# Performance work log

Hardware: AMD Instinct MI355X
Metric: run time of the kernel (lower is better)

## Reference

```python
import jax, jax.numpy as jnp
import numpy as np

B, N = 256, 256


def greedy_hard_perm(soft_perm):
    # soft_perm: (B, N, N). Sequential greedy masked-argmax assignment, vectorized over batch.
    Bn, Nn, _ = soft_perm.shape
    NEG = jnp.finfo(soft_perm.dtype).min
    b_idx = jnp.arange(Bn)

    def step(carry, _):
        scores, hard, row_mask, col_mask = carry
        # mask out already-assigned rows/cols (in-place masked_fill_ in torch -> carried scores)
        scores = jnp.where(row_mask[:, :, None], NEG, scores)
        scores = jnp.where(col_mask[:, None, :], NEG, scores)
        flat_idx = jnp.argmax(scores.reshape(Bn, -1), axis=1)  # (B,)
        r = flat_idx // Nn
        c = flat_idx % Nn
        hard = hard.at[b_idx, r, c].set(1.0)
        row_mask = row_mask.at[b_idx, r].set(True)
        col_mask = col_mask.at[b_idx, c].set(True)
        return (scores, hard, row_mask, col_mask), None

    init = (
        soft_perm,
        jnp.zeros_like(soft_perm),
        jnp.zeros((Bn, Nn), dtype=bool),
        jnp.zeros((Bn, Nn), dtype=bool),
    )
    (_, hard, _, _), _ = jax.lax.scan(step, init, None, length=Nn)
    return hard


def setup_inputs() -> dict:
    key = jax.random.key(0)
    logits = jax.random.normal(key, (B, N, N), dtype=jnp.float32)
    # realistic soft permutation: row-stochastic scores
    soft_perm = jax.nn.softmax(logits, axis=-1)
    return {"soft_perm": soft_perm}


def reference(soft_perm):
    # hard perm carries no gradient (built from constant 1.0 writes in torch)
    hard = greedy_hard_perm(jax.lax.stop_gradient(soft_perm))
    # straight-through estimator: forward = hard, backward = identity through soft
    return hard + soft_perm - jax.lax.stop_gradient(soft_perm)
```

## Files before the change

kernel.cpp:

```cpp
#include <hip/hip_runtime.h>
#include <math.h>

#define NEGINF (-INFINITY)
#define NEGINF_BITS ((int)0xFF800000)

typedef unsigned int u32;
typedef unsigned long long u64;

#define RST 128

template <int CTRL>
__device__ __forceinline__ float dppmax(float x) {
    int xi = __float_as_int(x);
    int yi = __builtin_amdgcn_update_dpp(xi, xi, CTRL, 0xf, 0xf, false);
    return fmaxf(x, __int_as_float(yi));
}

__device__ __forceinline__ float wave_max64(float x) {
    x = dppmax<0x111>(x);
    x = dppmax<0x112>(x);
    x = dppmax<0x114>(x);
    x = dppmax<0x118>(x);
    x = dppmax<0x142>(x);
    x = dppmax<0x143>(x);
    return __int_as_float(__builtin_amdgcn_readlane(__float_as_int(x), 63));
}

__device__ __forceinline__ void wave_argmax(float v, int idx, float& out_v, int& out_idx) {
    float mv = wave_max64(v);
    u64 mask = __ballot(v == mv);
    int ln = (int)__builtin_ctzll(mask);
    int bi = __builtin_amdgcn_readlane(idx, ln);
    u64 rest = mask & (mask - 1);
    if (rest) {
        while (rest) {
            int l2 = (int)__builtin_ctzll(rest); rest &= rest - 1;
            int b2 = __builtin_amdgcn_readlane(idx, l2);
            if (b2 < bi) bi = b2;
        }
    }
    out_v = mv; out_idx = bi;
}

__device__ __forceinline__ void wave_top2(float lv, int lf, float lv2, int lf2,
                                          float& nv, int& nc, float& nv2, int& nc2) {
    float av = lv, bv = lv2;
#define T2STAGE(CTRL) {                                                        \
        float a2 = __int_as_float(__builtin_amdgcn_update_dpp(                 \
            NEGINF_BITS, __float_as_int(av), CTRL, 0xf, 0xf, false));          \
        float b2 = __int_as_float(__builtin_amdgcn_update_dpp(                 \
            NEGINF_BITS, __float_as_int(bv), CTRL, 0xf, 0xf, false));          \
        float t = fminf(av, a2);                                               \
        av = fmaxf(av, a2);                                                    \
        bv = fmaxf(fmaxf(bv, b2), t); }
    T2STAGE(0x111) T2STAGE(0x112) T2STAGE(0x114) T2STAGE(0x118)
    T2STAGE(0x142) T2STAGE(0x143)
#undef T2STAGE
    nv = __int_as_float(__builtin_amdgcn_readlane(__float_as_int(av), 63));
    float sv = __int_as_float(__builtin_amdgcn_readlane(__float_as_int(bv), 63));

    u64 m1 = __ballot(lv == nv);
    int ln = (int)__builtin_ctzll(m1);
    nc = __builtin_amdgcn_readlane(lf, ln);

    nv2 = sv; nc2 = 300;
    if (sv > 0.f) {
        if (sv == nv) {
            int b2i = __builtin_amdgcn_readlane(__float_as_int(lv2), ln);
            if (__int_as_float(b2i) == nv) {
                nc2 = __builtin_amdgcn_readlane(lf2, ln);
            } else {
                u64 rest = m1 & (m1 - 1);
                int l2 = (int)__builtin_ctzll(rest);
                nc2 = __builtin_amdgcn_readlane(lf, l2);
            }
        } else {
            u64 m2 = __ballot(lv == sv || lv2 == sv);
            int l2 = (int)__builtin_ctzll(m2);
            int tli = __builtin_amdgcn_readlane(__float_as_int(lv), l2);
            nc2 = (__int_as_float(tli) == sv)
                      ? __builtin_amdgcn_readlane(lf, l2)
                      : __builtin_amdgcn_readlane(lf2, l2);
        }
    }
}

template <int RSTT>
__global__ __launch_bounds__(64, 1) void greedy_perm_kernel(
        const float* __restrict__ soft, float* __restrict__ out) {
    extern __shared__ float smem[];
    const int b = blockIdx.x;
    const int lane = threadIdx.x;
    const size_t base = (size_t)b << 16;
    const float* sc = soft + base;
    float* ob = out + base;

    float rv[4], sv[4];
    int   rc[4], scc[4];
#pragma unroll
    for (int j = 0; j < 4; ++j) { rv[j] = NEGINF; rc[j] = 0; sv[j] = NEGINF; scc[j] = 300; }

    const float4 zero4 = make_float4(0.f, 0.f, 0.f, 0.f);

    for (int k = 0; k < 64; k += 4) {
        float4 w[4][4];
#pragma unroll
        for (int j = 0; j < 4; ++j) {
            const float4* rp = (const float4*)(sc + (size_t)(j * 64 + lane) * 256);
#pragma unroll
            for (int kk = 0; kk < 4; ++kk) w[j][kk] = rp[k + kk];
        }
#pragma unroll
        for (int j = 0; j < 4; ++j) {
            float4* op = (float4*)(ob + (size_t)(j * 64 + lane) * 256);
#pragma unroll
            for (int kk = 0; kk < 4; ++kk) op[k + kk] = zero4;
        }
        if (RSTT > 0) {
#pragma unroll
            for (int j = 0; j < 2; ++j) {
                float* lp = &smem[(j * 64 + lane) << 8];
#pragma unroll
                for (int kk = 0; kk < 4; ++kk)
                    *(float4*)&lp[((k + kk) ^ lane) << 2] = w[j][kk];
            }
        }
#pragma unroll
        for (int j = 0; j < 4; ++j) {
#pragma unroll
            for (int kk = 0; kk < 4; ++kk) {
                const float4 ww = w[j][kk];
                const int bc = 4 * (k + kk);
                const float e[4] = {ww.x, ww.y, ww.z, ww.w};
#pragma unroll
                for (int q = 0; q < 4; ++q) {
                    const float x = e[q];
                    const int   cx = bc + q;
                    const bool g1 = x > rv[j];
                    const bool g2 = x > sv[j];
                    sv[j]  = g1 ? rv[j] : (g2 ? x  : sv[j]);
                    scc[j] = g1 ? rc[j] : (g2 ? cx : scc[j]);
                    rv[j]  = g1 ? x  : rv[j];
                    rc[j]  = g1 ? cx : rc[j];
                }
            }
        }
    }

    __threadfence_block();

    u32 colmask = 0;

    for (int step = 0; step < 256; ++step) {
        float bv = rv[0];
        int   bf = (lane << 8) | (rc[0] & 255);
#pragma unroll
        for (int j = 1; j < 4; ++j) {
            if (rv[j] > bv) { bv = rv[j]; bf = (((j << 6) + lane) << 8) | (rc[j] & 255); }
        }
        float gv; int gf;
        wave_argmax(bv, bf, gv, gf);
        (void)gv;
        const int r  = gf >> 8;
        const int cc = gf & 255;

        if (lane == 0) ob[gf] = 1.0f;
        if (lane == (r & 63)) {
            const int rj = r >> 6;
#pragma unroll
            for (int j = 0; j < 4; ++j) if (j == rj) { rv[j] = NEGINF; rc[j] = 300; }
        }
        if (lane == (cc >> 2)) colmask |= 1u << (cc & 3);

#pragma unroll
        for (int j = 0; j < 4; ++j) if (scc[j] == cc) scc[j] = 300;

        bool dd[4]; bool anyd = false;
#pragma unroll
        for (int j = 0; j < 4; ++j) { dd[j] = (rc[j] == cc); anyd |= dd[j]; }
        if (__ballot(anyd)) {
#pragma unroll
            for (int j = 0; j < 4; ++j) {
                const bool need = dd[j] && (scc[j] == 300);
                if (dd[j] && !need) {
                    rv[j] = sv[j]; rc[j] = scc[j];
                    sv[j] = NEGINF; scc[j] = 300;
                }
                u64 m = __ballot(need);
                while (m) {
                    const int ln = (int)__builtin_ctzll(m); m &= m - 1;
                    const int row = (j << 6) + ln;
                    float4 w = (RSTT > 0 && row < RSTT)
                        ? *(const float4*)&smem[(row << 8) | (((lane ^ ln) & 63) << 2)]
                        : *(const float4*)(sc + ((size_t)row << 8) + (lane << 2));
                    const float q0 = (colmask & 1u) ? NEGINF : w.x;
                    const float q1 = (colmask & 2u) ? NEGINF : w.y;
                    const float q2 = (colmask & 4u) ? NEGINF : w.z;
                    const float q3 = (colmask & 8u) ? NEGINF : w.w;
                    const int cb = lane << 2;
                    float lv = q0; int lf = cb;
                    float lv2 = NEGINF; int lf2 = cb;
                    {
                        bool g1 = q1 > lv, g2 = q1 > lv2;
                        lv2 = g1 ? lv : (g2 ? q1 : lv2); lf2 = g1 ? lf : (g2 ? cb + 1 : lf2);
                        lv  = g1 ? q1 : lv;              lf  = g1 ? cb + 1 : lf;
                        g1 = q2 > lv; g2 = q2 > lv2;
                        lv2 = g1 ? lv : (g2 ? q2 : lv2); lf2 = g1 ? lf : (g2 ? cb + 2 : lf2);
                        lv  = g1 ? q2 : lv;              lf  = g1 ? cb + 2 : lf;
                        g1 = q3 > lv; g2 = q3 > lv2;
                        lv2 = g1 ? lv : (g2 ? q3 : lv2); lf2 = g1 ? lf : (g2 ? cb + 3 : lf2);
                        lv  = g1 ? q3 : lv;              lf  = g1 ? cb + 3 : lf;
                    }
                    float nv, nv2; int nc, nc2;
                    wave_top2(lv, lf, lv2, lf2, nv, nc, nv2, nc2);
                    if (lane == ln) {
#pragma unroll
                        for (int jj = 0; jj < 4; ++jj) if (jj == j) {
                            rv[jj] = nv; rc[jj] = nc;
                            sv[jj] = nv2; scc[jj] = nc2;
                        }
                    }
                }
            }
        }
    }
}

extern "C" void kernel_launch(void* const* d_in, const int* in_sizes, int n_in,
                              void* d_out, int out_size, void* d_ws, size_t ws_size,
                              hipStream_t stream) {
    const float* soft = (const float*)d_in[0];
    float* out = (float*)d_out;
    const int n_batches = in_sizes[0] >> 16;

    static int use_lds = -1;
    if (use_lds < 0) {
        hipError_t e = hipFuncSetAttribute(
            reinterpret_cast<const void*>(greedy_perm_kernel<RST>),
            hipFuncAttributeMaxDynamicSharedMemorySize, RST * 256 * 4);
        use_lds = (e == hipSuccess) ? 1 : 0;
    }
    if (use_lds)
        greedy_perm_kernel<RST><<<n_batches, 64, RST * 256 * 4, stream>>>(soft, out);
    else
        greedy_perm_kernel<0><<<n_batches, 64, 0, stream>>>(soft, out);
}
```

Baseline: 293.2 us.

## Assign two greedy picks per step via wave top-2 when provably safe

Each greedy step now takes a wave-wide top-2 of the per-row maxima rather than a plain argmax. When the runner-up lies in a different column, is positive and has no tie with a row invalidated by the first pick, both assignments are committed in one iteration. This roughly halves the number of serial reduction rounds. Row rescans are also batched per lane through a need-mask. It adds more complex tie handling and a correctness risk if the safety condition is incomplete.

```diff
diff --git a/kernel.cpp b/kernel.cpp
--- a/kernel.cpp
+++ b/kernel.cpp
@@ -9,37 +9,11 @@
 
 #define RST 128
 
-template <int CTRL>
-__device__ __forceinline__ float dppmax(float x) {
-    int xi = __float_as_int(x);
-    int yi = __builtin_amdgcn_update_dpp(xi, xi, CTRL, 0xf, 0xf, false);
-    return fmaxf(x, __int_as_float(yi));
-}
-
-__device__ __forceinline__ float wave_max64(float x) {
-    x = dppmax<0x111>(x);
-    x = dppmax<0x112>(x);
-    x = dppmax<0x114>(x);
-    x = dppmax<0x118>(x);
-    x = dppmax<0x142>(x);
-    x = dppmax<0x143>(x);
-    return __int_as_float(__builtin_amdgcn_readlane(__float_as_int(x), 63));
-}
-
-__device__ __forceinline__ void wave_argmax(float v, int idx, float& out_v, int& out_idx) {
-    float mv = wave_max64(v);
-    u64 mask = __ballot(v == mv);
-    int ln = (int)__builtin_ctzll(mask);
-    int bi = __builtin_amdgcn_readlane(idx, ln);
-    u64 rest = mask & (mask - 1);
-    if (rest) {
-        while (rest) {
-            int l2 = (int)__builtin_ctzll(rest); rest &= rest - 1;
-            int b2 = __builtin_amdgcn_readlane(idx, l2);
-            if (b2 < bi) bi = b2;
-        }
-    }
-    out_v = mv; out_idx = bi;
+__device__ __forceinline__ int rl_i(int x, int l) {
+    return __builtin_amdgcn_readlane(x, l);
+}
+__device__ __forceinline__ float rl_f(float x, int l) {
+    return __int_as_float(__builtin_amdgcn_readlane(__float_as_int(x), l));
 }
 
 __device__ __forceinline__ void wave_top2(float lv, int lf, float lv2, int lf2,
@@ -56,31 +30,95 @@
     T2STAGE(0x111) T2STAGE(0x112) T2STAGE(0x114) T2STAGE(0x118)
     T2STAGE(0x142) T2STAGE(0x143)
 #undef T2STAGE
-    nv = __int_as_float(__builtin_amdgcn_readlane(__float_as_int(av), 63));
-    float sv = __int_as_float(__builtin_amdgcn_readlane(__float_as_int(bv), 63));
+    nv = rl_f(av, 63);
+    float sv = rl_f(bv, 63);
 
     u64 m1 = __ballot(lv == nv);
     int ln = (int)__builtin_ctzll(m1);
-    nc = __builtin_amdgcn_readlane(lf, ln);
+    nc = rl_i(lf, ln);
 
     nv2 = sv; nc2 = 300;
     if (sv > 0.f) {
         if (sv == nv) {
-            int b2i = __builtin_amdgcn_readlane(__float_as_int(lv2), ln);
-            if (__int_as_float(b2i) == nv) {
-                nc2 = __builtin_amdgcn_readlane(lf2, ln);
+            float b2v = rl_f(lv2, ln);
+            if (b2v == nv) {
+                nc2 = rl_i(lf2, ln);
             } else {
                 u64 rest = m1 & (m1 - 1);
                 int l2 = (int)__builtin_ctzll(rest);
-                nc2 = __builtin_amdgcn_readlane(lf, l2);
+                nc2 = rl_i(lf, l2);
             }
         } else {
             u64 m2 = __ballot(lv == sv || lv2 == sv);
             int l2 = (int)__builtin_ctzll(m2);
-            int tli = __builtin_amdgcn_readlane(__float_as_int(lv), l2);
-            nc2 = (__int_as_float(tli) == sv)
-                      ? __builtin_amdgcn_readlane(lf, l2)
-                      : __builtin_amdgcn_readlane(lf2, l2);
+            float tl = rl_f(lv, l2);
+            nc2 = (tl == sv) ? rl_i(lf, l2) : rl_i(lf2, l2);
+        }
+    }
+}
+
+__device__ __forceinline__ void wave_top2_flat(float lv, int lf, float lv2, int lf2,
+                                               float& nv, int& nf, float& sv, int& sf) {
+    float av = lv, bv = lv2;
+#define T2STAGE(CTRL) {                                                        \
+        float a2 = __int_as_float(__builtin_amdgcn_update_dpp(                 \
+            NEGINF_BITS, __float_as_int(av), CTRL, 0xf, 0xf, false));          \
+        float b2 = __int_as_float(__builtin_amdgcn_update_dpp(                 \
+            NEGINF_BITS, __float_as_int(bv), CTRL, 0xf, 0xf, false));          \
+        float t = fminf(av, a2);                                               \
+        av = fmaxf(av, a2);                                                    \
+        bv = fmaxf(fmaxf(bv, b2), t); }
+    T2STAGE(0x111) T2STAGE(0x112) T2STAGE(0x114) T2STAGE(0x118)
+    T2STAGE(0x142) T2STAGE(0x143)
+#undef T2STAGE
+    nv = rl_f(av, 63);
+    sv = rl_f(bv, 63);
+
+    u64 m1 = __ballot(lv == nv);
+    int ln = (int)__builtin_ctzll(m1);
+    nf = rl_i(lf, ln);
+    u64 rest = m1 & (m1 - 1);
+    if (rest) {
+        while (rest) {
+            int l2 = (int)__builtin_ctzll(rest); rest &= rest - 1;
+            int f = rl_i(lf, l2);
+            if (f < nf) nf = f;
+        }
+    }
+
+    sf = 0x7FFFFFFF;
+    if (sv > 0.f) {
+        if (sv == nv) {
+            int best = 0x7FFFFFFF;
+            u64 mm = m1;
+            while (mm) {
+                int l2 = (int)__builtin_ctzll(mm); mm &= mm - 1;
+                int f = rl_i(lf, l2);
+                if (f != nf && f < best) best = f;
+                float v2 = rl_f(lv2, l2);
+                if (v2 == nv) {
+                    int g = rl_i(lf2, l2);
+                    if (g != nf && g < best) best = g;
+                }
+            }
+            sf = best;
+        } else {
+            u64 m2 = __ballot(lv == sv || lv2 == sv);
+            u64 rest2 = m2 & (m2 - 1);
+            int l2 = (int)__builtin_ctzll(m2);
+            if (!rest2) {
+                float tl = rl_f(lv, l2);
+                sf = (tl == sv) ? rl_i(lf, l2) : rl_i(lf2, l2);
+            } else {
+                int best = 0x7FFFFFFF;
+                while (m2) {
+                    int l3 = (int)__builtin_ctzll(m2); m2 &= m2 - 1;
+                    float tl = rl_f(lv, l3);
+                    int f = (tl == sv) ? rl_i(lf, l3) : rl_i(lf2, l3);
+                    if (f < best) best = f;
+                }
+                sf = best;
+            }
         }
     }
 }
@@ -95,10 +133,10 @@
     const float* sc = soft + base;
     float* ob = out + base;
 
-    float rv[4], sv[4];
-    int   rc[4], scc[4];
-#pragma unroll
-    for (int j = 0; j < 4; ++j) { rv[j] = NEGINF; rc[j] = 0; sv[j] = NEGINF; scc[j] = 300; }
+    float rv[4], spv[4];
+    int   rc[4], spc[4];
+#pragma unroll
+    for (int j = 0; j < 4; ++j) { rv[j] = NEGINF; rc[j] = 0; spv[j] = NEGINF; spc[j] = 300; }
 
     const float4 zero4 = make_float4(0.f, 0.f, 0.f, 0.f);
 
@@ -137,9 +175,9 @@
                     const float x = e[q];
                     const int   cx = bc + q;
                     const bool g1 = x > rv[j];
-                    const bool g2 = x > sv[j];
-                    sv[j]  = g1 ? rv[j] : (g2 ? x  : sv[j]);
-                    scc[j] = g1 ? rc[j] : (g2 ? cx : scc[j]);
+                    const bool g2 = x > spv[j];
+                    spv[j] = g1 ? rv[j] : (g2 ? x  : spv[j]);
+                    spc[j] = g1 ? rc[j] : (g2 ? cx : spc[j]);
                     rv[j]  = g1 ? x  : rv[j];
                     rc[j]  = g1 ? cx : rc[j];
                 }
@@ -151,78 +189,114 @@
 
     u32 colmask = 0;
 
-    for (int step = 0; step < 256; ++step) {
+    int step = 0;
+    while (step < 256) {
         float bv = rv[0];
         int   bf = (lane << 8) | (rc[0] & 255);
+        float bv2 = NEGINF;
+        int   bf2 = bf;
 #pragma unroll
         for (int j = 1; j < 4; ++j) {
-            if (rv[j] > bv) { bv = rv[j]; bf = (((j << 6) + lane) << 8) | (rc[j] & 255); }
-        }
-        float gv; int gf;
-        wave_argmax(bv, bf, gv, gf);
-        (void)gv;
-        const int r  = gf >> 8;
-        const int cc = gf & 255;
+            const float v = rv[j];
+            const int   f = (((j << 6) + lane) << 8) | (rc[j] & 255);
+            const bool g1 = v > bv, g2 = v > bv2;
+            bv2 = g1 ? bv : (g2 ? v : bv2);
+            bf2 = g1 ? bf : (g2 ? f : bf2);
+            bv  = g1 ? v : bv;
+            bf  = g1 ? f : bf;
+        }
+        float nv, svv; int gf, f2;
+        wave_top2_flat(bv, bf, bv2, bf2, nv, gf, svv, f2);
+        const int r1 = gf >> 8;
+        const int c1 = gf & 255;
 
         if (lane == 0) ob[gf] = 1.0f;
-        if (lane == (r & 63)) {
-            const int rj = r >> 6;
+        if (lane == (r1 & 63)) {
+            const int rj = r1 >> 6;
 #pragma unroll
             for (int j = 0; j < 4; ++j) if (j == rj) { rv[j] = NEGINF; rc[j] = 300; }
         }
-        if (lane == (cc >> 2)) colmask |= 1u << (cc & 3);
-
-#pragma unroll
-        for (int j = 0; j < 4; ++j) if (scc[j] == cc) scc[j] = 300;
-
-        bool dd[4]; bool anyd = false;
-#pragma unroll
-        for (int j = 0; j < 4; ++j) { dd[j] = (rc[j] == cc); anyd |= dd[j]; }
-        if (__ballot(anyd)) {
-#pragma unroll
-            for (int j = 0; j < 4; ++j) {
-                const bool need = dd[j] && (scc[j] == 300);
-                if (dd[j] && !need) {
-                    rv[j] = sv[j]; rc[j] = scc[j];
-                    sv[j] = NEGINF; scc[j] = 300;
-                }
-                u64 m = __ballot(need);
-                while (m) {
-                    const int ln = (int)__builtin_ctzll(m); m &= m - 1;
-                    const int row = (j << 6) + ln;
-                    float4 w = (RSTT > 0 && row < RSTT)
-                        ? *(const float4*)&smem[(row << 8) | (((lane ^ ln) & 63) << 2)]
-                        : *(const float4*)(sc + ((size_t)row << 8) + (lane << 2));
-                    const float q0 = (colmask & 1u) ? NEGINF : w.x;
-                    const float q1 = (colmask & 2u) ? NEGINF : w.y;
-                    const float q2 = (colmask & 4u) ? NEGINF : w.z;
-                    const float q3 = (colmask & 8u) ? NEGINF : w.w;
-                    const int cb = lane << 2;
-                    float lv = q0; int lf = cb;
-                    float lv2 = NEGINF; int lf2 = cb;
-                    {
-                        bool g1 = q1 > lv, g2 = q1 > lv2;
-                        lv2 = g1 ? lv : (g2 ? q1 : lv2); lf2 = g1 ? lf : (g2 ? cb + 1 : lf2);
-                        lv  = g1 ? q1 : lv;              lf  = g1 ? cb + 1 : lf;
-                        g1 = q2 > lv; g2 = q2 > lv2;
-                        lv2 = g1 ? lv : (g2 ? q2 : lv2); lf2 = g1 ? lf : (g2 ? cb + 2 : lf2);
-                        lv  = g1 ? q2 : lv;              lf  = g1 ? cb + 2 : lf;
-                        g1 = q3 > lv; g2 = q3 > lv2;
-                        lv2 = g1 ? lv : (g2 ? q3 : lv2); lf2 = g1 ? lf : (g2 ? cb + 3 : lf2);
-                        lv  = g1 ? q3 : lv;              lf  = g1 ? cb + 3 : lf;
+        if (lane == (c1 >> 2)) colmask |= 1u << (c1 & 3);
+
+        bool dd1[4]; bool tie = false;
+#pragma unroll
+        for (int j = 0; j < 4; ++j) {
+            dd1[j] = (rc[j] == c1);
+            tie |= dd1[j] && (rv[j] == svv);
+        }
+        const u64 tb = __ballot(tie);
+        const bool use2 = (svv > 0.f) && ((f2 & 255) != c1) && (tb == 0ull);
+
+        int c2 = -1;
+        if (use2) {
+            const int r2 = f2 >> 8;
+            c2 = f2 & 255;
+            if (lane == 0) ob[f2] = 1.0f;
+            if (lane == (r2 & 63)) {
+                const int rj = r2 >> 6;
+#pragma unroll
+                for (int j = 0; j < 4; ++j) if (j == rj) { rv[j] = NEGINF; rc[j] = 300; }
+            }
+            if (lane == (c2 >> 2)) colmask |= 1u << (c2 & 3);
+        }
+
+#pragma unroll
+        for (int j = 0; j < 4; ++j)
+            if (spc[j] == c1 || spc[j] == c2) spc[j] = 300;
+
+        u32 needmask = 0;
+#pragma unroll
+        for (int j = 0; j < 4; ++j) {
+            const bool dirty = dd1[j] || (rc[j] == c2);
+            const bool have  = (spc[j] < 300);
+            if (dirty && have) {
+                rv[j] = spv[j]; rc[j] = spc[j];
+                spv[j] = NEGINF; spc[j] = 300;
+            }
+            if (dirty && !have) needmask |= 1u << j;
+        }
+
+        u64 nb = __ballot(needmask != 0);
+        while (nb) {
+            const int l = (int)__builtin_ctzll(nb); nb &= nb - 1;
+            u32 nm = (u32)rl_i((int)needmask, l);
+            while (nm) {
+                const int j = (int)__builtin_ctzll(nm); nm &= nm - 1;
+                const int row = (j << 6) + l;
+                float4 w = (RSTT > 0 && row < RSTT)
+                    ? *(const float4*)&smem[(row << 8) | (((lane ^ l) & 63) << 2)]
+                    : *(const float4*)(sc + ((size_t)row << 8) + (lane << 2));
+                const float q0 = (colmask & 1u) ? NEGINF : w.x;
+                const float q1 = (colmask & 2u) ? NEGINF : w.y;
+                const float q2 = (colmask & 4u) ? NEGINF : w.z;
+                const float q3 = (colmask & 8u) ? NEGINF : w.w;
+                const int cb = lane << 2;
+                float lv = q0; int lf = cb;
+                float lv2 = NEGINF; int lf2 = cb;
+                {
+                    bool g1 = q1 > lv, g2 = q1 > lv2;
+                    lv2 = g1 ? lv : (g2 ? q1 : lv2); lf2 = g1 ? lf : (g2 ? cb + 1 : lf2);
+                    lv  = g1 ? q1 : lv;              lf  = g1 ? cb + 1 : lf;
+                    g1 = q2 > lv; g2 = q2 > lv2;
+                    lv2 = g1 ? lv : (g2 ? q2 : lv2); lf2 = g1 ? lf : (g2 ? cb + 2 : lf2);
+                    lv  = g1 ? q2 : lv;              lf  = g1 ? cb + 2 : lf;
+                    g1 = q3 > lv; g2 = q3 > lv2;
+                    lv2 = g1 ? lv : (g2 ? q3 : lv2); lf2 = g1 ? lf : (g2 ? cb + 3 : lf2);
+                    lv  = g1 ? q3 : lv;              lf  = g1 ? cb + 3 : lf;
+                }
+                float fv, fv2; int fc, fc2;
+                wave_top2(lv, lf, lv2, lf2, fv, fc, fv2, fc2);
+                if (lane == l) {
+#pragma unroll
+                    for (int jj = 0; jj < 4; ++jj) if (jj == j) {
+                        rv[jj] = fv; rc[jj] = fc;
+                        spv[jj] = fv2; spc[jj] = fc2;
                     }
-                    float nv, nv2; int nc, nc2;
-                    wave_top2(lv, lf, lv2, lf2, nv, nc, nv2, nc2);
-                    if (lane == ln) {
-#pragma unroll
-                        for (int jj = 0; jj < 4; ++jj) if (jj == j) {
-                            rv[jj] = nv; rc[jj] = nc;
-                            sv[jj] = nv2; scc[jj] = nc2;
-                        }
-                    }
-                }
-            }
-        }
+                }
+            }
+        }
+
+        step += use2 ? 2 : 1;
     }
 }
 
```

After: 307.2 us. 4.8% more time.

## Interleave row ownership per lane and fuse argmax value-index DPP reduction

Applied to the files above, without the earlier changes.

Rows are now owned as lane*4+j instead of j*64+lane, so the packed argmax index encodes the owner lane and slot directly. The wave argmax carries the flat index through the DPP reduction instead of doing a max, a ballot and a tie loop. Rows that need a rescan are collected into a per-lane bitmask and walked lane by lane. The aim is to shorten the serial per-step critical path. The change also alters the LDS staging pattern, and tie-breaking with >= in the DPP chain may pick a different index than the reference on equal values.

```diff
diff --git a/kernel.cpp b/kernel.cpp
--- a/kernel.cpp
+++ b/kernel.cpp
@@ -9,37 +9,24 @@
 
 #define RST 128
 
-template <int CTRL>
-__device__ __forceinline__ float dppmax(float x) {
-    int xi = __float_as_int(x);
-    int yi = __builtin_amdgcn_update_dpp(xi, xi, CTRL, 0xf, 0xf, false);
-    return fmaxf(x, __int_as_float(yi));
-}
-
-__device__ __forceinline__ float wave_max64(float x) {
-    x = dppmax<0x111>(x);
-    x = dppmax<0x112>(x);
-    x = dppmax<0x114>(x);
-    x = dppmax<0x118>(x);
-    x = dppmax<0x142>(x);
-    x = dppmax<0x143>(x);
-    return __int_as_float(__builtin_amdgcn_readlane(__float_as_int(x), 63));
-}
-
-__device__ __forceinline__ void wave_argmax(float v, int idx, float& out_v, int& out_idx) {
-    float mv = wave_max64(v);
-    u64 mask = __ballot(v == mv);
-    int ln = (int)__builtin_ctzll(mask);
-    int bi = __builtin_amdgcn_readlane(idx, ln);
-    u64 rest = mask & (mask - 1);
-    if (rest) {
-        while (rest) {
-            int l2 = (int)__builtin_ctzll(rest); rest &= rest - 1;
-            int b2 = __builtin_amdgcn_readlane(idx, l2);
-            if (b2 < bi) bi = b2;
-        }
-    }
-    out_v = mv; out_idx = bi;
+__device__ __forceinline__ int rl_i(int x, int l) {
+    return __builtin_amdgcn_readlane(x, l);
+}
+__device__ __forceinline__ float rl_f(float x, int l) {
+    return __int_as_float(__builtin_amdgcn_readlane(__float_as_int(x), l));
+}
+
+__device__ __forceinline__ int wave_argmax_flat(float v, int f) {
+#define AIX(CTRL) {                                                            \
+        float vin = __int_as_float(__builtin_amdgcn_update_dpp(                \
+            __float_as_int(v), __float_as_int(v), CTRL, 0xf, 0xf, false));     \
+        int fin = __builtin_amdgcn_update_dpp(f, f, CTRL, 0xf, 0xf, false);    \
+        const bool c = vin >= v;                                               \
+        v = c ? vin : v;                                                       \
+        f = c ? fin : f; }
+    AIX(0x111) AIX(0x112) AIX(0x114) AIX(0x118) AIX(0x142) AIX(0x143)
+#undef AIX
+    return rl_i(f, 63);
 }
 
 __device__ __forceinline__ void wave_top2(float lv, int lf, float lv2, int lf2,
@@ -56,31 +43,29 @@
     T2STAGE(0x111) T2STAGE(0x112) T2STAGE(0x114) T2STAGE(0x118)
     T2STAGE(0x142) T2STAGE(0x143)
 #undef T2STAGE
-    nv = __int_as_float(__builtin_amdgcn_readlane(__float_as_int(av), 63));
-    float sv = __int_as_float(__builtin_amdgcn_readlane(__float_as_int(bv), 63));
+    nv = rl_f(av, 63);
+    float sv = rl_f(bv, 63);
 
     u64 m1 = __ballot(lv == nv);
     int ln = (int)__builtin_ctzll(m1);
-    nc = __builtin_amdgcn_readlane(lf, ln);
+    nc = rl_i(lf, ln);
 
     nv2 = sv; nc2 = 300;
     if (sv > 0.f) {
         if (sv == nv) {
-            int b2i = __builtin_amdgcn_readlane(__float_as_int(lv2), ln);
-            if (__int_as_float(b2i) == nv) {
-                nc2 = __builtin_amdgcn_readlane(lf2, ln);
+            float b2v = rl_f(lv2, ln);
+            if (b2v == nv) {
+                nc2 = rl_i(lf2, ln);
             } else {
                 u64 rest = m1 & (m1 - 1);
                 int l2 = (int)__builtin_ctzll(rest);
-                nc2 = __builtin_amdgcn_readlane(lf, l2);
+                nc2 = rl_i(lf, l2);
             }
         } else {
             u64 m2 = __ballot(lv == sv || lv2 == sv);
             int l2 = (int)__builtin_ctzll(m2);
-            int tli = __builtin_amdgcn_readlane(__float_as_int(lv), l2);
-            nc2 = (__int_as_float(tli) == sv)
-                      ? __builtin_amdgcn_readlane(lf, l2)
-                      : __builtin_amdgcn_readlane(lf2, l2);
+            float tl = rl_f(lv, l2);
+            nc2 = (tl == sv) ? rl_i(lf, l2) : rl_i(lf2, l2);
         }
     }
 }
@@ -95,10 +80,10 @@
     const float* sc = soft + base;
     float* ob = out + base;
 
-    float rv[4], sv[4];
-    int   rc[4], scc[4];
-#pragma unroll
-    for (int j = 0; j < 4; ++j) { rv[j] = NEGINF; rc[j] = 0; sv[j] = NEGINF; scc[j] = 300; }
+    float rv[4], spv[4];
+    int   rc[4], spc[4];
+#pragma unroll
+    for (int j = 0; j < 4; ++j) { rv[j] = NEGINF; rc[j] = 0; spv[j] = NEGINF; spc[j] = 300; }
 
     const float4 zero4 = make_float4(0.f, 0.f, 0.f, 0.f);
 
@@ -106,23 +91,23 @@
         float4 w[4][4];
 #pragma unroll
         for (int j = 0; j < 4; ++j) {
-            const float4* rp = (const float4*)(sc + (size_t)(j * 64 + lane) * 256);
+            const float4* rp = (const float4*)(sc + (size_t)(4 * lane + j) * 256);
 #pragma unroll
             for (int kk = 0; kk < 4; ++kk) w[j][kk] = rp[k + kk];
         }
 #pragma unroll
         for (int j = 0; j < 4; ++j) {
-            float4* op = (float4*)(ob + (size_t)(j * 64 + lane) * 256);
+            float4* op = (float4*)(ob + (size_t)(4 * lane + j) * 256);
 #pragma unroll
             for (int kk = 0; kk < 4; ++kk) op[k + kk] = zero4;
         }
-        if (RSTT > 0) {
-#pragma unroll
-            for (int j = 0; j < 2; ++j) {
-                float* lp = &smem[(j * 64 + lane) << 8];
+        if (RSTT > 0 && lane < (RSTT >> 2)) {
+#pragma unroll
+            for (int j = 0; j < 4; ++j) {
+                float* lp = &smem[(4 * lane + j) << 8];
 #pragma unroll
                 for (int kk = 0; kk < 4; ++kk)
-                    *(float4*)&lp[((k + kk) ^ lane) << 2] = w[j][kk];
+                    *(float4*)&lp[(((k + kk) ^ lane) & 63) << 2] = w[j][kk];
             }
         }
 #pragma unroll
@@ -137,9 +122,9 @@
                     const float x = e[q];
                     const int   cx = bc + q;
                     const bool g1 = x > rv[j];
-                    const bool g2 = x > sv[j];
-                    sv[j]  = g1 ? rv[j] : (g2 ? x  : sv[j]);
-                    scc[j] = g1 ? rc[j] : (g2 ? cx : scc[j]);
+                    const bool g2 = x > spv[j];
+                    spv[j] = g1 ? rv[j] : (g2 ? x  : spv[j]);
+                    spc[j] = g1 ? rc[j] : (g2 ? cx : spc[j]);
                     rv[j]  = g1 ? x  : rv[j];
                     rc[j]  = g1 ? cx : rc[j];
                 }
@@ -153,72 +138,74 @@
 
     for (int step = 0; step < 256; ++step) {
         float bv = rv[0];
-        int   bf = (lane << 8) | (rc[0] & 255);
+        int   bf = (lane << 10) | (rc[0] & 255);
 #pragma unroll
         for (int j = 1; j < 4; ++j) {
-            if (rv[j] > bv) { bv = rv[j]; bf = (((j << 6) + lane) << 8) | (rc[j] & 255); }
-        }
-        float gv; int gf;
-        wave_argmax(bv, bf, gv, gf);
-        (void)gv;
-        const int r  = gf >> 8;
-        const int cc = gf & 255;
+            if (rv[j] > bv) { bv = rv[j]; bf = (lane << 10) | (j << 8) | (rc[j] & 255); }
+        }
+        const int gf = wave_argmax_flat(bv, bf);
+        const int cc    = gf & 255;
+        const int owner = gf >> 10;
+        const int rj    = (gf >> 8) & 3;
 
         if (lane == 0) ob[gf] = 1.0f;
-        if (lane == (r & 63)) {
-            const int rj = r >> 6;
-#pragma unroll
-            for (int j = 0; j < 4; ++j) if (j == rj) { rv[j] = NEGINF; rc[j] = 300; }
-        }
         if (lane == (cc >> 2)) colmask |= 1u << (cc & 3);
-
-#pragma unroll
-        for (int j = 0; j < 4; ++j) if (scc[j] == cc) scc[j] = 300;
-
-        bool dd[4]; bool anyd = false;
-#pragma unroll
-        for (int j = 0; j < 4; ++j) { dd[j] = (rc[j] == cc); anyd |= dd[j]; }
-        if (__ballot(anyd)) {
-#pragma unroll
-            for (int j = 0; j < 4; ++j) {
-                const bool need = dd[j] && (scc[j] == 300);
-                if (dd[j] && !need) {
-                    rv[j] = sv[j]; rc[j] = scc[j];
-                    sv[j] = NEGINF; scc[j] = 300;
-                }
-                u64 m = __ballot(need);
-                while (m) {
-                    const int ln = (int)__builtin_ctzll(m); m &= m - 1;
-                    const int row = (j << 6) + ln;
-                    float4 w = (RSTT > 0 && row < RSTT)
-                        ? *(const float4*)&smem[(row << 8) | (((lane ^ ln) & 63) << 2)]
-                        : *(const float4*)(sc + ((size_t)row << 8) + (lane << 2));
-                    const float q0 = (colmask & 1u) ? NEGINF : w.x;
-                    const float q1 = (colmask & 2u) ? NEGINF : w.y;
-                    const float q2 = (colmask & 4u) ? NEGINF : w.z;
-                    const float q3 = (colmask & 8u) ? NEGINF : w.w;
-                    const int cb = lane << 2;
-                    float lv = q0; int lf = cb;
-                    float lv2 = NEGINF; int lf2 = cb;
-                    {
-                        bool g1 = q1 > lv, g2 = q1 > lv2;
-                        lv2 = g1 ? lv : (g2 ? q1 : lv2); lf2 = g1 ? lf : (g2 ? cb + 1 : lf2);
-                        lv  = g1 ? q1 : lv;              lf  = g1 ? cb + 1 : lf;
-                        g1 = q2 > lv; g2 = q2 > lv2;
-                        lv2 = g1 ? lv : (g2 ? q2 : lv2); lf2 = g1 ? lf : (g2 ? cb + 2 : lf2);
-                        lv  = g1 ? q2 : lv;              lf  = g1 ? cb + 2 : lf;
-                        g1 = q3 > lv; g2 = q3 > lv2;
-                        lv2 = g1 ? lv : (g2 ? q3 : lv2); lf2 = g1 ? lf : (g2 ? cb + 3 : lf2);
-                        lv  = g1 ? q3 : lv;              lf  = g1 ? cb + 3 : lf;
-                    }
-                    float nv, nv2; int nc, nc2;
-                    wave_top2(lv, lf, lv2, lf2, nv, nc, nv2, nc2);
-                    if (lane == ln) {
-#pragma unroll
-                        for (int jj = 0; jj < 4; ++jj) if (jj == j) {
-                            rv[jj] = nv; rc[jj] = nc;
-                            sv[jj] = nv2; scc[jj] = nc2;
-                        }
+        const bool iown = (lane == owner);
+
+        u32 needmask = 0;
+#pragma unroll
+        for (int j = 0; j < 4; ++j) {
+            if (spc[j] == cc) spc[j] = 300;
+            const bool match = (rc[j] == cc);
+            if (match) {
+                const bool win  = iown && (j == rj);
+                const bool have = (spc[j] < 300);
+                if (win) {
+                    rv[j] = NEGINF; rc[j] = 300;
+                } else if (have) {
+                    rv[j] = spv[j]; rc[j] = spc[j];
+                    spv[j] = NEGINF; spc[j] = 300;
+                } else {
+                    needmask |= 1u << j;
+                }
+            }
+        }
+
+        u64 nb = __ballot(needmask != 0);
+        while (nb) {
+            const int l = (int)__builtin_ctzll(nb); nb &= nb - 1;
+            u32 nm = (u32)rl_i((int)needmask, l);
+            while (nm) {
+                const int j = (int)__builtin_ctzll(nm); nm &= nm - 1;
+                const int row = (l << 2) + j;
+                float4 w = (RSTT > 0 && row < RSTT)
+                    ? *(const float4*)&smem[(row << 8) | (((lane ^ l) & 63) << 2)]
+                    : *(const float4*)(sc + ((size_t)row << 8) + (lane << 2));
+                const float q0 = (colmask & 1u) ? NEGINF : w.x;
+                const float q1 = (colmask & 2u) ? NEGINF : w.y;
+                const float q2 = (colmask & 4u) ? NEGINF : w.z;
+                const float q3 = (colmask & 8u) ? NEGINF : w.w;
+                const int cb = lane << 2;
+                float lv = q0; int lf = cb;
+                float lv2 = NEGINF; int lf2 = cb;
+                {
+                    bool g1 = q1 > lv, g2 = q1 > lv2;
+                    lv2 = g1 ? lv : (g2 ? q1 : lv2); lf2 = g1 ? lf : (g2 ? cb + 1 : lf2);
+                    lv  = g1 ? q1 : lv;              lf  = g1 ? cb + 1 : lf;
+                    g1 = q2 > lv; g2 = q2 > lv2;
+                    lv2 = g1 ? lv : (g2 ? q2 : lv2); lf2 = g1 ? lf : (g2 ? cb + 2 : lf2);
+                    lv  = g1 ? q2 : lv;              lf  = g1 ? cb + 2 : lf;
+                    g1 = q3 > lv; g2 = q3 > lv2;
+                    lv2 = g1 ? lv : (g2 ? q3 : lv2); lf2 = g1 ? lf : (g2 ? cb + 3 : lf2);
+                    lv  = g1 ? q3 : lv;              lf  = g1 ? cb + 3 : lf;
+                }
+                float fv, fv2; int fc, fc2;
+                wave_top2(lv, lf, lv2, lf2, fv, fc, fv2, fc2);
+                if (lane == l) {
+#pragma unroll
+                    for (int jj = 0; jj < 4; ++jj) if (jj == j) {
+                        rv[jj] = fv; rc[jj] = fc;
+                        spv[jj] = fv2; spc[jj] = fc2;
                     }
                 }
             }
@@ -233,14 +220,10 @@
     float* out = (float*)d_out;
     const int n_batches = in_sizes[0] >> 16;
 
-    static int use_lds = -1;
-    if (use_lds < 0) {
-        hipError_t e = hipFuncSetAttribute(
-            reinterpret_cast<const void*>(greedy_perm_kernel<RST>),
-            hipFuncAttributeMaxDynamicSharedMemorySize, RST * 256 * 4);
-        use_lds = (e == hipSuccess) ? 1 : 0;
-    }
-    if (use_lds)
+    hipError_t e = hipFuncSetAttribute(
+        reinterpret_cast<const void*>(greedy_perm_kernel<RST>),
+        hipFuncAttributeMaxDynamicSharedMemorySize, RST * 256 * 4);
+    if (e == hipSuccess)
         greedy_perm_kernel<RST><<<n_batches, 64, RST * 256 * 4, stream>>>(soft, out);
     else
         greedy_perm_kernel<0><<<n_batches, 64, 0, stream>>>(soft, out);
```

Measured after the change: 322.0 us. +9.8%, slower.
